# Kernel optimization log

Hardware: AMD Instinct MI355X
Metric: run time of the kernel (lower is better)

The kernel has to match this reference:

```python
import jax, jax.numpy as jnp
import numpy as np


def setup_inputs() -> dict:
    key = jax.random.key(0)
    k1, k2 = jax.random.split(key)
    B, C, H, W_ = 16, 512, 64, 64
    x = jax.random.normal(k1, (B, C, H, W_), dtype=jnp.float32)
    W = jax.random.normal(k2, (C, C), dtype=jnp.float32) * (1.0 / np.sqrt(C))
    return {"x": x, "W": W}


def reference(x, W):
    B, C, H, Wd = x.shape
    hw = H * Wd
    x1 = x.reshape(B, C, hw)                      # [B, C, HW]
    # linearW applied to x1^T: [B, HW, C] @ W^T -> [B, HW, C]
    x1_corr = jnp.einsum('bch,dc->bhd', x1, W)    # [B, HW, C]
    s = jnp.einsum('bch,bhd->bcd', x1, x1_corr)   # [B, C, C]
    a = jax.nn.softmax(s, axis=2)
    a = jax.nn.softmax(a, axis=1)
    out = jnp.einsum('bcd,bdh->bch', a, x1) + x1  # [B, C, HW]
    return out.reshape(B, C, H, Wd)
```

## Files before the change

### kernel.cpp

```cpp
#include <hip/hip_runtime.h>


typedef __attribute__((ext_vector_type(8))) short bf16x8;
typedef __attribute__((ext_vector_type(4))) float f32x4;

#define DEVINL __device__ __forceinline__
#define CFENCE() asm volatile("" ::: "memory")

DEVINL unsigned short f2bf(float f) {
  union { float f; unsigned int u; } c; c.f = f;
  unsigned int u = c.u;
  u += 0x7fffu + ((u >> 16) & 1u);
  return (unsigned short)(u >> 16);
}

DEVINL float bf2f(unsigned short h) {
  union { unsigned int u; float f; } c; c.u = ((unsigned int)h) << 16;
  return c.f;
}

DEVINL void gld_lds16(const unsigned short* g, unsigned short* l) {
  __builtin_amdgcn_global_load_lds(
      (const __attribute__((address_space(1))) unsigned int*)g,
      (__attribute__((address_space(3))) unsigned int*)l,
      16 , 0, 0);
}

template<int N> DEVINL void vm_wait() {
  if constexpr (N == 0)       asm volatile("s_waitcnt vmcnt(0)" ::: "memory");
  else if constexpr (N == 2)  asm volatile("s_waitcnt vmcnt(2)" ::: "memory");
  else if constexpr (N == 4)  asm volatile("s_waitcnt vmcnt(4)" ::: "memory");
  else if constexpr (N == 6)  asm volatile("s_waitcnt vmcnt(6)" ::: "memory");
  else if constexpr (N == 8)  asm volatile("s_waitcnt vmcnt(8)" ::: "memory");
  else static_assert(N < 0, "unsupported vmcnt");
}

DEVINL void lgkm0() { asm volatile("s_waitcnt lgkmcnt(0)" ::: "memory"); }

DEVINL void sym_tile_decode(int t, int& tm, int& tn) {
  if (t < 4)      { tm = 0; tn = t; }
  else if (t < 7) { tm = 1; tn = t - 3; }
  else if (t < 9) { tm = 2; tn = t - 5; }
  else            { tm = 3; tn = 3; }
}

__global__ __launch_bounds__(256)
void cvt_kernel(const float* __restrict__ in, unsigned short* __restrict__ out, int n4) {
  int i = blockIdx.x * 256 + threadIdx.x;
  const int stride = gridDim.x * 256;
  for (; i < n4; i += stride) {
    float4 v = ((const float4*)in)[i];
    unsigned int lo = (unsigned int)f2bf(v.x) | ((unsigned int)f2bf(v.y) << 16);
    unsigned int hi = (unsigned int)f2bf(v.z) | ((unsigned int)f2bf(v.w) << 16);
    uint2 o; o.x = lo; o.y = hi;
    ((uint2*)out)[i] = o;
  }
}

__global__ __launch_bounds__(256)
void gemm_gsym(const unsigned short* __restrict__ X, unsigned short* __restrict__ P) {
  constexpr int HALF = 128 * 32;
  __shared__ unsigned short As[2 * HALF];
  __shared__ unsigned short Bs[2 * HALF];
  const int tid = threadIdx.x;
  const int l   = tid & 63;
  const int w   = tid >> 6;
  const int wr  = w >> 1, wc = w & 1;
  const int b   = blockIdx.y;
  const int t   = blockIdx.x >> 2;
  const int split = blockIdx.x & 3;
  int tm, tn; sym_tile_decode(t, tm, tn);

  const unsigned short* Ab = X + (long long)b * 2097152 + (long long)(tm * 128) * 4096;
  const unsigned short* Bb = X + (long long)b * 2097152 + (long long)(tn * 128) * 4096;

  f32x4 acc[4][4];
  #pragma unroll
  for (int m = 0; m < 4; ++m)
    #pragma unroll
    for (int n = 0; n < 4; ++n) acc[m][n] = (f32x4){0.f, 0.f, 0.f, 0.f};

  const int srow = tid >> 2;
  const int scol = ((tid & 3) ^ ((tid >> 3) & 3)) * 8;
  const int ch8  = (((l >> 4) ^ ((l >> 1) & 3)) * 8);

  auto stage = [&](int buf, int k0) {
    #pragma unroll
    for (int i = 0; i < 2; ++i)
      gld_lds16(Ab + (long long)(i * 64 + srow) * 4096 + k0 + scol, &As[buf * HALF + i * 2048 + tid * 8]);
    #pragma unroll
    for (int i = 0; i < 2; ++i)
      gld_lds16(Bb + (long long)(i * 64 + srow) * 4096 + k0 + scol, &Bs[buf * HALF + i * 2048 + tid * 8]);
  };
  auto compute = [&](int buf) {
    bf16x8 af[4], bfr[4];
    #pragma unroll
    for (int m = 0; m < 4; ++m)
      af[m] = *(const bf16x8*)&As[buf * HALF + (wr * 64 + m * 16 + (l & 15)) * 32 + ch8];
    #pragma unroll
    for (int n = 0; n < 4; ++n)
      bfr[n] = *(const bf16x8*)&Bs[buf * HALF + (wc * 64 + n * 16 + (l & 15)) * 32 + ch8];
    __builtin_amdgcn_s_setprio(1);
    #pragma unroll
    for (int m = 0; m < 4; ++m)
      #pragma unroll
      for (int n = 0; n < 4; ++n)
        acc[m][n] = __builtin_amdgcn_mfma_f32_16x16x32_bf16(af[m], bfr[n], acc[m][n], 0, 0, 0);
    __builtin_amdgcn_s_setprio(0);
  };

  const int k_beg = split * 1024;
  constexpr int NK = 32;
  stage(0, k_beg);
  stage(1, k_beg + 32);
  int ks = k_beg + 64;
  for (int k = 0; k < NK - 2; ++k) {
    vm_wait<4>();
    CFENCE(); __builtin_amdgcn_s_barrier(); CFENCE();
    compute(k & 1);
    CFENCE(); __builtin_amdgcn_s_barrier(); CFENCE();
    stage(k & 1, ks); ks += 32;
  }
  vm_wait<4>();
  CFENCE(); __builtin_amdgcn_s_barrier(); CFENCE();
  compute((NK - 2) & 1);
  vm_wait<0>();
  CFENCE(); __builtin_amdgcn_s_barrier(); CFENCE();
  compute((NK - 1) & 1);

  unsigned short* Pt = P + (((long long)b * 10 + t) * 4 + split) * 16384;
  const int cc = l & 15, r4 = (l >> 4) * 4;
  #pragma unroll
  for (int m = 0; m < 4; ++m) {
    #pragma unroll
    for (int n = 0; n < 4; ++n) {
      const int row = wr * 64 + m * 16 + r4;
      const int col = wc * 64 + n * 16 + cc;
      #pragma unroll
      for (int j = 0; j < 4; ++j)
        Pt[(row + j) * 128 + col] = f2bf(acc[m][n][j]);
    }
  }
}

__global__ __launch_bounds__(256)
void reduce_mirror(const unsigned short* __restrict__ P, unsigned short* __restrict__ G) {
  __shared__ unsigned short T[128 * 129];
  const int tid = threadIdx.x;
  const int b = blockIdx.y;
  const int t = blockIdx.x;
  int tm, tn; sym_tile_decode(t, tm, tn);
  const unsigned short* Pt = P + ((long long)(b * 10 + t) * 4) * 16384;
  unsigned short* Gb = G + (long long)b * 262144;

  #pragma unroll
  for (int e = 0; e < 16; ++e) {
    const int v = e * 256 + tid;
    ushort4 s0 = ((const ushort4*)Pt)[v];
    ushort4 s1 = ((const ushort4*)(Pt + 16384))[v];
    ushort4 s2 = ((const ushort4*)(Pt + 32768))[v];
    ushort4 s3 = ((const ushort4*)(Pt + 49152))[v];
    unsigned int h0 = f2bf(bf2f(s0.x) + bf2f(s1.x) + bf2f(s2.x) + bf2f(s3.x));
    unsigned int h1 = f2bf(bf2f(s0.y) + bf2f(s1.y) + bf2f(s2.y) + bf2f(s3.y));
    unsigned int h2 = f2bf(bf2f(s0.z) + bf2f(s1.z) + bf2f(s2.z) + bf2f(s3.z));
    unsigned int h3 = f2bf(bf2f(s0.w) + bf2f(s1.w) + bf2f(s2.w) + bf2f(s3.w));
    const int idx = v * 4;
    const int r = idx >> 7, c = idx & 127;
    unsigned int* gp = (unsigned int*)(Gb + (long long)(tm * 128 + r) * 512 + tn * 128 + c);
    gp[0] = h0 | (h1 << 16);
    gp[1] = h2 | (h3 << 16);
    unsigned short* tp = &T[r * 129 + c];
    tp[0] = (unsigned short)h0; tp[1] = (unsigned short)h1;
    tp[2] = (unsigned short)h2; tp[3] = (unsigned short)h3;
  }
  if (tm != tn) {
    __syncthreads();
    #pragma unroll
    for (int e = 0; e < 16; ++e) {
      const int idx = (e * 256 + tid) * 4;
      const int r = idx >> 7, c = idx & 127;
      unsigned int o0 = T[(c + 0) * 129 + r], o1 = T[(c + 1) * 129 + r];
      unsigned int o2 = T[(c + 2) * 129 + r], o3 = T[(c + 3) * 129 + r];
      unsigned int* gp = (unsigned int*)(Gb + (long long)(tn * 128 + r) * 512 + tm * 128 + c);
      gp[0] = o0 | (o1 << 16);
      gp[1] = o2 | (o3 << 16);
    }
  }
}

__global__ __launch_bounds__(256)
void gemm_s(const unsigned short* __restrict__ A, const unsigned short* __restrict__ B,
            float* __restrict__ C) {
  constexpr int HALF = 64 * 32;
  __shared__ unsigned short As[2 * HALF];
  __shared__ unsigned short Bs[2 * HALF];

  const int tid = threadIdx.x;
  const int l   = tid & 63;
  const int w   = tid >> 6;
  const int wr  = w >> 1, wc = w & 1;
  const int bz  = blockIdx.y;
  const int tm  = blockIdx.x >> 3;
  const int tn  = blockIdx.x & 7;

  const unsigned short* Ab = A + (long long)bz * 262144 + (long long)(tm * 64) * 512;
  const unsigned short* Bb = B + (long long)(tn * 64) * 512;

  f32x4 acc[2][2];
  #pragma unroll
  for (int m = 0; m < 2; ++m)
    #pragma unroll
    for (int n = 0; n < 2; ++n) acc[m][n] = (f32x4){0.f, 0.f, 0.f, 0.f};

  const int srow = tid >> 2;
  const int scol = ((tid & 3) ^ ((tid >> 3) & 3)) * 8;
  const int ch8  = (((l >> 4) ^ ((l >> 1) & 3)) * 8);

  auto stage = [&](int buf, int k0) {
    gld_lds16(Ab + (long long)srow * 512 + k0 + scol, &As[buf * HALF + tid * 8]);
    gld_lds16(Bb + (long long)srow * 512 + k0 + scol, &Bs[buf * HALF + tid * 8]);
  };
  auto compute = [&](int buf) {
    bf16x8 af[2], bfr[2];
    #pragma unroll
    for (int m = 0; m < 2; ++m)
      af[m] = *(const bf16x8*)&As[buf * HALF + (wr * 32 + m * 16 + (l & 15)) * 32 + ch8];
    #pragma unroll
    for (int n = 0; n < 2; ++n)
      bfr[n] = *(const bf16x8*)&Bs[buf * HALF + (wc * 32 + n * 16 + (l & 15)) * 32 + ch8];
    __builtin_amdgcn_s_setprio(1);
    #pragma unroll
    for (int m = 0; m < 2; ++m)
      #pragma unroll
      for (int n = 0; n < 2; ++n)
        acc[m][n] = __builtin_amdgcn_mfma_f32_16x16x32_bf16(af[m], bfr[n], acc[m][n], 0, 0, 0);
    __builtin_amdgcn_s_setprio(0);
  };

  stage(0, 0);
  stage(1, 32);
  int ks = 64;
  for (int k = 0; k < 14; ++k) {
    vm_wait<2>();
    CFENCE(); __builtin_amdgcn_s_barrier(); CFENCE();
    compute(k & 1);
    CFENCE(); __builtin_amdgcn_s_barrier(); CFENCE();
    stage(k & 1, ks); ks += 32;
  }
  vm_wait<2>();
  CFENCE(); __builtin_amdgcn_s_barrier(); CFENCE();
  compute(0);
  vm_wait<0>();
  CFENCE(); __builtin_amdgcn_s_barrier(); CFENCE();
  compute(1);

  const int cc = l & 15, r4 = (l >> 4) * 4;
  const int row0 = tm * 64 + wr * 32;
  const int col0 = tn * 64 + wc * 32;
  #pragma unroll
  for (int m = 0; m < 2; ++m) {
    #pragma unroll
    for (int n = 0; n < 2; ++n) {
      const int row = row0 + m * 16 + r4;
      const int col = col0 + n * 16 + cc;
      long long base = (long long)bz * 262144 + (long long)row * 512 + col;
      #pragma unroll
      for (int j = 0; j < 4; ++j)
        C[base + (long long)j * 512] = acc[m][n][j];
    }
  }
}

__global__ __launch_bounds__(256)
void gemm_out(const unsigned short* __restrict__ A, const unsigned short* __restrict__ X,
              float* __restrict__ C) {
  __shared__ unsigned short As[2][128 * 32];
  __shared__ unsigned int   Bs[2][16][132];

  const int tid = threadIdx.x;
  const int l   = tid & 63;
  const int w   = tid >> 6;
  const int wr  = w >> 1, wc = w & 1;
  const int bz  = blockIdx.y;
  const int tm  = blockIdx.x >> 5;
  const int tn  = blockIdx.x & 31;

  const unsigned short* Ab = A + (long long)bz * 262144  + (long long)(tm * 128) * 512;
  const unsigned short* Xb = X + (long long)bz * 2097152 + tn * 128;

  f32x4 acc[4][4];
  #pragma unroll
  for (int m = 0; m < 4; ++m)
    #pragma unroll
    for (int n = 0; n < 4; ++n) acc[m][n] = (f32x4){0.f, 0.f, 0.f, 0.f};

  const int srow = tid >> 2;
  const int scol = ((tid & 3) ^ ((tid >> 3) & 3)) * 8;
  const int ch8  = (((l >> 4) ^ ((l >> 1) & 3)) * 8);
  const int bp_  = tid >> 4;
  const int bh_  = tid & 15;
  const unsigned short* Bsrc = Xb + (long long)(2 * bp_) * 4096 + bh_ * 8;

  auto Agload = [&](int buf, int k0) {
    #pragma unroll
    for (int i = 0; i < 2; ++i)
      gld_lds16(Ab + (long long)(i * 64 + srow) * 512 + k0 + scol, &As[buf][i * 2048 + tid * 8]);
  };
  auto Bload = [&](int k0, uint4& g0, uint4& g1) {
    g0 = *(const uint4*)(Bsrc + (long long)k0 * 4096);
    g1 = *(const uint4*)(Bsrc + (long long)(k0 + 1) * 4096);
  };
  auto Bdswrite = [&](int buf, const uint4& g0, const uint4& g1) {
    unsigned int w0 = (g0.x & 0xffffu) | (g1.x << 16);
    unsigned int w1 = (g0.x >> 16)    | (g1.x & 0xffff0000u);
    unsigned int w2 = (g0.y & 0xffffu) | (g1.y << 16);
    unsigned int w3 = (g0.y >> 16)    | (g1.y & 0xffff0000u);
    unsigned int w4 = (g0.z & 0xffffu) | (g1.z << 16);
    unsigned int w5 = (g0.z >> 16)    | (g1.z & 0xffff0000u);
    unsigned int w6 = (g0.w & 0xffffu) | (g1.w << 16);
    unsigned int w7 = (g0.w >> 16)    | (g1.w & 0xffff0000u);
    unsigned int* dst = &Bs[buf][bp_][bh_ * 8];
    uint4 o0; o0.x = w0; o0.y = w1; o0.z = w2; o0.w = w3;
    uint4 o1; o1.x = w4; o1.y = w5; o1.z = w6; o1.w = w7;
    *(uint4*)dst = o0;
    *(uint4*)(dst + 4) = o1;
  };
  auto compute = [&](int buf) {
    bf16x8 af[4], bfr[4];
    #pragma unroll
    for (int m = 0; m < 4; ++m)
      af[m] = *(const bf16x8*)&As[buf][(wr * 64 + m * 16 + (l & 15)) * 32 + ch8];
    const int hl = wc * 64 + (l & 15);
    const int p0 = (l >> 4) * 4;
    #pragma unroll
    for (int n = 0; n < 4; ++n) {
      unsigned int wv[4];
      #pragma unroll
      for (int i = 0; i < 4; ++i) wv[i] = Bs[buf][p0 + i][hl + n * 16];
      bfr[n] = *(bf16x8*)wv;
    }
    __builtin_amdgcn_s_setprio(1);
    #pragma unroll
    for (int m = 0; m < 4; ++m)
      #pragma unroll
      for (int n = 0; n < 4; ++n)
        acc[m][n] = __builtin_amdgcn_mfma_f32_16x16x32_bf16(af[m], bfr[n], acc[m][n], 0, 0, 0);
    __builtin_amdgcn_s_setprio(0);
  };

  uint4 e0, e1, o0, o1;
  Bload(0, e0, e1);
  Agload(0, 0);
  Bload(32, o0, o1);
  Agload(1, 32);
  vm_wait<6>();
  Bdswrite(0, e0, e1);
  lgkm0();
  CFENCE(); __builtin_amdgcn_s_barrier(); CFENCE();

  #pragma unroll 1
  for (int kk = 0; kk < 7; ++kk) {
    const int k = 2 * kk;
    vm_wait<4>();
    compute(0);
    vm_wait<2>();
    Bdswrite(1, o0, o1);
    lgkm0();
    CFENCE(); __builtin_amdgcn_s_barrier(); CFENCE();
    Bload((k + 2) * 32, e0, e1);
    Agload(0, (k + 2) * 32);
    vm_wait<4>();
    compute(1);
    vm_wait<2>();
    Bdswrite(0, e0, e1);
    lgkm0();
    CFENCE(); __builtin_amdgcn_s_barrier(); CFENCE();
    Bload((k + 3) * 32, o0, o1);
    Agload(1, (k + 3) * 32);
  }
  vm_wait<4>();
  compute(0);
  vm_wait<0>();
  Bdswrite(1, o0, o1);
  lgkm0();
  CFENCE(); __builtin_amdgcn_s_barrier(); CFENCE();
  compute(1);

  const int cc = l & 15, r4 = (l >> 4) * 4;
  const int row0 = tm * 128 + wr * 64;
  const int col0 = tn * 128 + wc * 64;
  #pragma unroll
  for (int m = 0; m < 4; ++m) {
    #pragma unroll
    for (int n = 0; n < 4; ++n) {
      const int row = row0 + m * 16 + r4;
      const int col = col0 + n * 16 + cc;
      long long base = (long long)bz * 2097152 + (long long)row * 4096 + col;
      #pragma unroll
      for (int j = 0; j < 4; ++j)
        __builtin_nontemporal_store(acc[m][n][j], &C[base + (long long)j * 4096]);
    }
  }
}

__global__ __launch_bounds__(256)
void row_softmax_kernel(const float* __restrict__ s, unsigned short* __restrict__ p_bf) {
  __shared__ float red[4], red2[4];
  const float* p = s + (long long)blockIdx.x * 512;
  unsigned short* q = p_bf + (long long)blockIdx.x * 512;
  const int tid = threadIdx.x;
  float v0 = p[tid], v1 = p[tid + 256];
  float m = fmaxf(v0, v1);
  #pragma unroll
  for (int i = 1; i < 64; i <<= 1) m = fmaxf(m, __shfl_xor(m, i));
  if ((tid & 63) == 0) red[tid >> 6] = m;
  __syncthreads();
  m = fmaxf(fmaxf(red[0], red[1]), fmaxf(red[2], red[3]));
  float e0 = __expf(v0 - m), e1 = __expf(v1 - m);
  float sum = e0 + e1;
  #pragma unroll
  for (int i = 1; i < 64; i <<= 1) sum += __shfl_xor(sum, i);
  if ((tid & 63) == 0) red2[tid >> 6] = sum;
  __syncthreads();
  sum = (red2[0] + red2[1]) + (red2[2] + red2[3]);
  float inv = 1.0f / sum;
  q[tid] = f2bf(e0 * inv);
  q[tid + 256] = f2bf(e1 * inv);
}

__global__ __launch_bounds__(256)
void col_softmax_kernel(const unsigned short* __restrict__ p_bf, unsigned short* __restrict__ a_bf) {
  __shared__ float cs[8][32];
  const int tid = threadIdx.x;
  const int dl = tid & 31;
  const int st = tid >> 5;
  const int d  = blockIdx.x * 32 + dl;
  const long long base = (long long)blockIdx.y * 262144 + d;
  const unsigned short* p = p_bf + base;
  float sum = 0.f;
  #pragma unroll 4
  for (int c = st * 64; c < st * 64 + 64; ++c)
    sum += __expf(bf2f(p[(long long)c * 512]));
  cs[st][dl] = sum;
  __syncthreads();
  if (st == 0) {
    float s = ((cs[0][dl] + cs[1][dl]) + (cs[2][dl] + cs[3][dl]))
            + ((cs[4][dl] + cs[5][dl]) + (cs[6][dl] + cs[7][dl]));
    cs[0][dl] = 1.0f / s;
  }
  __syncthreads();
  const float inv = cs[0][dl];
  unsigned short* q = a_bf + base;
  #pragma unroll 4
  for (int c = st * 64; c < st * 64 + 64; ++c) {
    float v = __expf(bf2f(p[(long long)c * 512])) * inv;
    if (c == d) v += 1.0f;
    q[(long long)c * 512] = f2bf(v);
  }
}

extern "C" void kernel_launch(void* const* d_in, const int* in_sizes, int n_in,
                              void* d_out, int out_size, void* d_ws, size_t ws_size,
                              hipStream_t stream) {
  (void)in_sizes; (void)n_in; (void)out_size; (void)ws_size;
  const float* x = (const float*)d_in[0];
  const float* W = (const float*)d_in[1];
  float* out = (float*)d_out;
  char* ws = (char*)d_ws;

  unsigned short* P    = (unsigned short*)((char*)d_out + 67108864);
  unsigned short* p_bf = (unsigned short*)((char*)d_out + 88080384);

  unsigned short* x_bf = (unsigned short*)ws;
  unsigned short* G_bf = (unsigned short*)(ws + 67108864);
  float*          s_f  = (float*)(ws + 75497472);
  unsigned short* W_bf = (unsigned short*)(ws + 92274688);
  unsigned short* a_bf = G_bf;

  cvt_kernel<<<4096, 256, 0, stream>>>(x, x_bf, 8388608);
  cvt_kernel<<<256, 256, 0, stream>>>(W, W_bf, 65536);

  gemm_gsym<<<dim3(40, 16), 256, 0, stream>>>(x_bf, P);

  reduce_mirror<<<dim3(10, 16), 256, 0, stream>>>(P, G_bf);

  gemm_s<<<dim3(64, 16), 256, 0, stream>>>(G_bf, W_bf, s_f);

  row_softmax_kernel<<<8192, 256, 0, stream>>>(s_f, p_bf);
  col_softmax_kernel<<<dim3(16, 16), 256, 0, stream>>>(p_bf, a_bf);

  gemm_out<<<dim3(128, 16), 256, 0, stream>>>(a_bf, x_bf, out);
}
```

Baseline: 164.9 us.

## Fuse row-softmax stats into score GEMM epilogue and merge conversion kernels

The score GEMM epilogue now computes per-tile online-softmax partial max and sum-exp for each row and writes them to a small stats buffer. The separate row-softmax kernel is removed, and the column-softmax kernel rebuilds each row's log-sum-exp from those partials. It then reads the fp32 scores directly, keeping the intermediate probabilities in shared memory. The two fp32-to-bf16 conversion launches are merged into one kernel. The aim is to save a full pass over the score matrix and two launches, at the cost of more exp work and a larger shared-memory footprint in the column kernel.

```diff
diff --git a/kernel.cpp b/kernel.cpp
--- a/kernel.cpp
+++ b/kernel.cpp
@@ -31,7 +31,6 @@
   else if constexpr (N == 2)  asm volatile("s_waitcnt vmcnt(2)" ::: "memory");
   else if constexpr (N == 4)  asm volatile("s_waitcnt vmcnt(4)" ::: "memory");
   else if constexpr (N == 6)  asm volatile("s_waitcnt vmcnt(6)" ::: "memory");
-  else if constexpr (N == 8)  asm volatile("s_waitcnt vmcnt(8)" ::: "memory");
   else static_assert(N < 0, "unsupported vmcnt");
 }
 
@@ -45,15 +44,19 @@
 }
 
 __global__ __launch_bounds__(256)
-void cvt_kernel(const float* __restrict__ in, unsigned short* __restrict__ out, int n4) {
-  int i = blockIdx.x * 256 + threadIdx.x;
-  const int stride = gridDim.x * 256;
-  for (; i < n4; i += stride) {
-    float4 v = ((const float4*)in)[i];
+void cvt2_kernel(const float* __restrict__ x, unsigned short* __restrict__ x_bf,
+                 const float* __restrict__ Wm, unsigned short* __restrict__ W_bf) {
+  long long i = (long long)blockIdx.x * 256 + threadIdx.x;
+  const long long stride = (long long)gridDim.x * 256;
+  for (; i < 8454144; i += stride) {
+    const bool isX = (i < 8388608);
+    const long long j = isX ? i : (i - 8388608);
+    float4 v = isX ? ((const float4*)x)[j] : ((const float4*)Wm)[j];
     unsigned int lo = (unsigned int)f2bf(v.x) | ((unsigned int)f2bf(v.y) << 16);
     unsigned int hi = (unsigned int)f2bf(v.z) | ((unsigned int)f2bf(v.w) << 16);
     uint2 o; o.x = lo; o.y = hi;
-    ((uint2*)out)[i] = o;
+    if (isX) ((uint2*)x_bf)[j] = o;
+    else     ((uint2*)W_bf)[j] = o;
   }
 }
 
@@ -190,10 +193,11 @@
 
 __global__ __launch_bounds__(256)
 void gemm_s(const unsigned short* __restrict__ A, const unsigned short* __restrict__ B,
-            float* __restrict__ C) {
+            float* __restrict__ C, float* __restrict__ stats) {
   constexpr int HALF = 64 * 32;
   __shared__ unsigned short As[2 * HALF];
   __shared__ unsigned short Bs[2 * HALF];
+  __shared__ float sm[2][64], sl[2][64];
 
   const int tid = threadIdx.x;
   const int l   = tid & 63;
@@ -268,6 +272,103 @@
       for (int j = 0; j < 4; ++j)
         C[base + (long long)j * 512] = acc[m][n][j];
     }
+  }
+
+  float mv[2][4], lv[2][4];
+  #pragma unroll
+  for (int m = 0; m < 2; ++m)
+    #pragma unroll
+    for (int j = 0; j < 4; ++j) {
+      float v0 = acc[m][0][j], v1 = acc[m][1][j];
+      float mx = fmaxf(v0, v1);
+      mv[m][j] = mx;
+      lv[m][j] = __expf(v0 - mx) + __expf(v1 - mx);
+    }
+  #pragma unroll
+  for (int off = 1; off < 16; off <<= 1) {
+    #pragma unroll
+    for (int m = 0; m < 2; ++m)
+      #pragma unroll
+      for (int j = 0; j < 4; ++j) {
+        float om = __shfl_xor(mv[m][j], off);
+        float ol = __shfl_xor(lv[m][j], off);
+        float nm = fmaxf(mv[m][j], om);
+        lv[m][j] = lv[m][j] * __expf(mv[m][j] - nm) + ol * __expf(om - nm);
+        mv[m][j] = nm;
+      }
+  }
+  if ((l & 15) == 0) {
+    const int g = l >> 4;
+    #pragma unroll
+    for (int m = 0; m < 2; ++m)
+      #pragma unroll
+      for (int j = 0; j < 4; ++j) {
+        const int r = wr * 32 + m * 16 + g * 4 + j;
+        sm[wc][r] = mv[m][j];
+        sl[wc][r] = lv[m][j];
+      }
+  }
+  __syncthreads();
+  if (tid < 64) {
+    float m0 = sm[0][tid], l0 = sl[0][tid];
+    float m1 = sm[1][tid], l1 = sl[1][tid];
+    float M = fmaxf(m0, m1);
+    float L = l0 * __expf(m0 - M) + l1 * __expf(m1 - M);
+    float2 st; st.x = M; st.y = L;
+    ((float2*)stats)[((long long)bz * 512 + tm * 64 + tid) * 8 + tn] = st;
+  }
+}
+
+__global__ __launch_bounds__(256)
+void col_softmax_v2(const float* __restrict__ s, const float* __restrict__ stats,
+                    unsigned short* __restrict__ a_bf) {
+  __shared__ float lse[512];
+  __shared__ unsigned short pt[512][32];
+  __shared__ float cs[8][32];
+  const int tid = threadIdx.x;
+  const int b   = blockIdx.y;
+
+  #pragma unroll
+  for (int rr = 0; rr < 2; ++rr) {
+    const int r = tid + rr * 256;
+    const float2* pp = (const float2*)stats + ((long long)b * 512 + r) * 8;
+    float M = pp[0].x;
+    #pragma unroll
+    for (int q = 1; q < 8; ++q) M = fmaxf(M, pp[q].x);
+    float Z = 0.f;
+    #pragma unroll
+    for (int q = 0; q < 8; ++q) Z += pp[q].y * __expf(pp[q].x - M);
+    lse[r] = M + __logf(Z);
+  }
+  __syncthreads();
+
+  const int dl = tid & 31;
+  const int st = tid >> 5;
+  const int d  = blockIdx.x * 32 + dl;
+  const float* sp = s + (long long)b * 262144 + d;
+  float sum = 0.f;
+  #pragma unroll 4
+  for (int c = st * 64; c < st * 64 + 64; ++c) {
+    float p = __expf(sp[(long long)c * 512] - lse[c]);
+    float t = __expf(p);
+    pt[c][dl] = f2bf(t);
+    sum += t;
+  }
+  cs[st][dl] = sum;
+  __syncthreads();
+  if (st == 0) {
+    float tot = ((cs[0][dl] + cs[1][dl]) + (cs[2][dl] + cs[3][dl]))
+              + ((cs[4][dl] + cs[5][dl]) + (cs[6][dl] + cs[7][dl]));
+    cs[0][dl] = 1.0f / tot;
+  }
+  __syncthreads();
+  const float inv = cs[0][dl];
+  unsigned short* q = a_bf + (long long)b * 262144 + d;
+  #pragma unroll 4
+  for (int c = st * 64; c < st * 64 + 64; ++c) {
+    float v = bf2f(pt[c][dl]) * inv;
+    if (c == d) v += 1.0f;
+    q[(long long)c * 512] = f2bf(v);
   }
 }
 
@@ -403,62 +504,6 @@
   }
 }
 
-__global__ __launch_bounds__(256)
-void row_softmax_kernel(const float* __restrict__ s, unsigned short* __restrict__ p_bf) {
-  __shared__ float red[4], red2[4];
-  const float* p = s + (long long)blockIdx.x * 512;
-  unsigned short* q = p_bf + (long long)blockIdx.x * 512;
-  const int tid = threadIdx.x;
-  float v0 = p[tid], v1 = p[tid + 256];
-  float m = fmaxf(v0, v1);
-  #pragma unroll
-  for (int i = 1; i < 64; i <<= 1) m = fmaxf(m, __shfl_xor(m, i));
-  if ((tid & 63) == 0) red[tid >> 6] = m;
-  __syncthreads();
-  m = fmaxf(fmaxf(red[0], red[1]), fmaxf(red[2], red[3]));
-  float e0 = __expf(v0 - m), e1 = __expf(v1 - m);
-  float sum = e0 + e1;
-  #pragma unroll
-  for (int i = 1; i < 64; i <<= 1) sum += __shfl_xor(sum, i);
-  if ((tid & 63) == 0) red2[tid >> 6] = sum;
-  __syncthreads();
-  sum = (red2[0] + red2[1]) + (red2[2] + red2[3]);
-  float inv = 1.0f / sum;
-  q[tid] = f2bf(e0 * inv);
-  q[tid + 256] = f2bf(e1 * inv);
-}
-
-__global__ __launch_bounds__(256)
-void col_softmax_kernel(const unsigned short* __restrict__ p_bf, unsigned short* __restrict__ a_bf) {
-  __shared__ float cs[8][32];
-  const int tid = threadIdx.x;
-  const int dl = tid & 31;
-  const int st = tid >> 5;
-  const int d  = blockIdx.x * 32 + dl;
-  const long long base = (long long)blockIdx.y * 262144 + d;
-  const unsigned short* p = p_bf + base;
-  float sum = 0.f;
-  #pragma unroll 4
-  for (int c = st * 64; c < st * 64 + 64; ++c)
-    sum += __expf(bf2f(p[(long long)c * 512]));
-  cs[st][dl] = sum;
-  __syncthreads();
-  if (st == 0) {
-    float s = ((cs[0][dl] + cs[1][dl]) + (cs[2][dl] + cs[3][dl]))
-            + ((cs[4][dl] + cs[5][dl]) + (cs[6][dl] + cs[7][dl]));
-    cs[0][dl] = 1.0f / s;
-  }
-  __syncthreads();
-  const float inv = cs[0][dl];
-  unsigned short* q = a_bf + base;
-  #pragma unroll 4
-  for (int c = st * 64; c < st * 64 + 64; ++c) {
-    float v = __expf(bf2f(p[(long long)c * 512])) * inv;
-    if (c == d) v += 1.0f;
-    q[(long long)c * 512] = f2bf(v);
-  }
-}
-
 extern "C" void kernel_launch(void* const* d_in, const int* in_sizes, int n_in,
                               void* d_out, int out_size, void* d_ws, size_t ws_size,
                               hipStream_t stream) {
@@ -468,8 +513,8 @@
   float* out = (float*)d_out;
   char* ws = (char*)d_ws;
 
-  unsigned short* P    = (unsigned short*)((char*)d_out + 67108864);
-  unsigned short* p_bf = (unsigned short*)((char*)d_out + 88080384);
+  unsigned short* P = (unsigned short*)((char*)d_out + 67108864);
+  float* s_stats    = (float*)((char*)d_out + 67108864);
 
   unsigned short* x_bf = (unsigned short*)ws;
   unsigned short* G_bf = (unsigned short*)(ws + 67108864);
@@ -477,17 +522,15 @@
   unsigned short* W_bf = (unsigned short*)(ws + 92274688);
   unsigned short* a_bf = G_bf;
 
-  cvt_kernel<<<4096, 256, 0, stream>>>(x, x_bf, 8388608);
-  cvt_kernel<<<256, 256, 0, stream>>>(W, W_bf, 65536);
+  cvt2_kernel<<<4096, 256, 0, stream>>>(x, x_bf, W, W_bf);
 
   gemm_gsym<<<dim3(40, 16), 256, 0, stream>>>(x_bf, P);
 
   reduce_mirror<<<dim3(10, 16), 256, 0, stream>>>(P, G_bf);
 
-  gemm_s<<<dim3(64, 16), 256, 0, stream>>>(G_bf, W_bf, s_f);
-
-  row_softmax_kernel<<<8192, 256, 0, stream>>>(s_f, p_bf);
-  col_softmax_kernel<<<dim3(16, 16), 256, 0, stream>>>(p_bf, a_bf);
+  gemm_s<<<dim3(64, 16), 256, 0, stream>>>(G_bf, W_bf, s_f, s_stats);
+
+  col_softmax_v2<<<dim3(16, 16), 256, 0, stream>>>(s_f, s_stats, a_bf);
 
   gemm_out<<<dim3(128, 16), 256, 0, stream>>>(a_bf, x_bf, out);
 }
```

Result: faster. 161.4 us (-2.1%).
